# Kernel tuning notes

Hardware: AMD Instinct MI355X
Metric: run time of the kernel (lower is better)

The kernel has to match this reference:

```python
import jax, jax.numpy as jnp
import numpy as np

N, E, FIN, H, OUT, L = 80000, 1280000, 128, 64, 10, 3
NEG_SLOPE = 0.2


def setup_inputs() -> dict:
    key = jax.random.key(0)
    ks = jax.random.split(key, 2 + 6 * L + 2)
    inp = {
        "x": jax.random.normal(ks[0], (N, FIN), dtype=jnp.float32),
        "edge_index": jax.random.randint(ks[1], (2, E), 0, N, dtype=jnp.int32),
        "batch": jnp.zeros((N,), dtype=jnp.int32),
    }
    k = 2
    for l in range(L):
        fin = FIN if l == 0 else H
        s = 1.0 / np.sqrt(fin)
        inp[f"Wl{l}"] = jax.random.normal(ks[k + 0], (H, fin), dtype=jnp.float32) * s
        inp[f"bl{l}"] = jnp.zeros((H,), dtype=jnp.float32)
        inp[f"Wr{l}"] = jax.random.normal(ks[k + 1], (H, fin), dtype=jnp.float32) * s
        inp[f"br{l}"] = jnp.zeros((H,), dtype=jnp.float32)
        inp[f"att{l}"] = jax.random.normal(ks[k + 2], (H,), dtype=jnp.float32) * (1.0 / np.sqrt(H))
        inp[f"b{l}"] = jnp.zeros((H,), dtype=jnp.float32)
        k += 3
    inp["Wro"] = jax.random.normal(ks[k], (OUT, H), dtype=jnp.float32) * (1.0 / np.sqrt(H))
    inp["bro"] = jnp.zeros((OUT,), dtype=jnp.float32)
    return inp


def gatv2_layer(h, src, dst, Wl, bl, Wr, br, att, b):
    # PyG GATv2Conv (heads=1, share_weights=False):
    #   xl = lin_l(h) (source side), xr = lin_r(h) (target side)
    xl = h @ Wl.T + bl          # [N, H]
    xr = h @ Wr.T + br          # [N, H]
    e = jax.nn.leaky_relu(xl[src] + xr[dst], NEG_SLOPE) @ att  # [E_tot]
    # softmax over incoming edges of each destination node
    m = jax.ops.segment_max(e, dst, num_segments=N)
    ex = jnp.exp(e - m[dst])
    denom = jax.ops.segment_sum(ex, dst, num_segments=N)
    alpha = ex / denom[dst]
    out = jax.ops.segment_sum(alpha[:, None] * xl[src], dst, num_segments=N)
    return out + b


def reference(x, edge_index, batch,
              Wl0, bl0, Wr0, br0, att0, b0,
              Wl1, bl1, Wr1, br1, att1, b1,
              Wl2, bl2, Wr2, br2, att2, b2,
              Wro, bro):
    # add self-loops once (same augmented edge set used each layer)
    loop = jnp.arange(N, dtype=edge_index.dtype)
    src = jnp.concatenate([edge_index[0], loop])
    dst = jnp.concatenate([edge_index[1], loop])
    layers = [
        (Wl0, bl0, Wr0, br0, att0, b0),
        (Wl1, bl1, Wr1, br1, att1, b1),
        (Wl2, bl2, Wr2, br2, att2, b2),
    ]
    h = x
    for (Wl, bl, Wr, br, att, b) in layers:
        h = jax.nn.relu(gatv2_layer(h, src, dst, Wl, bl, Wr, br, att, b))
    # graph_level_task=False: node-level readout
    return h @ Wro.T + bro  # [N, OUT]
```

## Files before the change

kernel.cpp:

```cpp
#include <hip/hip_runtime.h>
#include <hip/hip_bf16.h>
#include <hip/hip_fp16.h>


#define NN 80000
#define EE 1280000
#define FIN 128
#define HH 64
#define OUTD 10
#define NBUK 79
#define PCH 2048
#define NCH 625

typedef __hip_bfloat16 bf16;
typedef _Float16 f16x8 __attribute__((ext_vector_type(8)));
typedef float f32x4 __attribute__((ext_vector_type(4)));

__device__ __forceinline__ float ldw(const void* p, int i, int f) {
    return f ? __bfloat162float(((const bf16*)p)[i]) : ((const float*)p)[i];
}

__global__ void detect_kernel(const unsigned* __restrict__ w, int* __restrict__ flag) {
    int lane = threadIdx.x;
    int big = 0;
    for (int i = lane; i < 2048; i += 64) {
        unsigned u = w[i];
        float a = __uint_as_float(u << 16);
        float b = __uint_as_float(u & 0xffff0000u);
        if (!(fabsf(a) <= 1024.f)) big = 1;
        if (!(fabsf(b) <= 1024.f)) big = 1;
    }
    big = (__ballot(big) != 0ull) ? 1 : 0;
    if (lane == 0) flag[0] = big ? 0 : 1;
}

__global__ void preconvert(
    const void* Wl0, const void* Wr0, const void* Wl1, const void* Wr1,
    const void* Wl2, const void* Wr2,
    const void* bl0, const void* br0, const void* bl1, const void* br1,
    const void* bl2, const void* br2,
    const void* att0, const void* att1, const void* att2,
    const void* b0, const void* b1, const void* b2,
    const void* Wro, const void* bro,
    __half* Wh0, __half* Wh1, __half* Wh2, float* small,
    const int* __restrict__ flagp)
{
    const int f = flagp[0];
    int t = blockIdx.x * 256 + threadIdx.x;
    if (t < 16384) {
        int j = t & 127, k = t >> 7;
        float v = (j < 64) ? ldw(Wl0, j * 128 + k, f) : ldw(Wr0, (j - 64) * 128 + k, f);
        Wh0[j * 128 + k] = __float2half(v);
    } else if (t < 24576) {
        int u = t - 16384; int j = u & 127, k = u >> 7;
        float v = (j < 64) ? ldw(Wl1, j * 64 + k, f) : ldw(Wr1, (j - 64) * 64 + k, f);
        Wh1[j * 64 + k] = __float2half(v);
    } else if (t < 32768) {
        int u = t - 24576; int j = u & 127, k = u >> 7;
        float v = (j < 64) ? ldw(Wl2, j * 64 + k, f) : ldw(Wr2, (j - 64) * 64 + k, f);
        Wh2[j * 64 + k] = __float2half(v);
    } else if (t < 34304) {
        int s = t - 32768;
        const void* BL[3] = { bl0, bl1, bl2 };
        const void* BR[3] = { br0, br1, br2 };
        const void* AT[3] = { att0, att1, att2 };
        const void* BB[3] = { b0, b1, b2 };
        float v = 0.f;
        if (s < 384) {
            int l = s / 128, r = s % 128;
            v = (r < 64) ? ldw(BL[l], r, f) : ldw(BR[l], r - 64, f);
        } else if (s < 576) {
            int q = s - 384; v = ldw(AT[q / 64], q % 64, f);
        } else if (s < 768) {
            int q = s - 576; v = ldw(BB[q / 64], q % 64, f);
        } else if (s < 1408) {
            v = ldw(Wro, s - 768, f);
        } else if (s < 1418) {
            v = ldw(bro, s - 1408, f);
        } else return;
        small[s] = v;
    }
}

__global__ __launch_bounds__(256) void chunkhist_kernel(const int* __restrict__ dst,
                                                        int* __restrict__ chunkcnt)
{
    __shared__ int h[NBUK];
    const int tid = threadIdx.x, c = blockIdx.x;
    for (int i = tid; i < NBUK; i += 256) h[i] = 0;
    __syncthreads();
    const int e0 = c * PCH + tid * 8;
    int4 a = *(const int4*)(dst + e0);
    int4 b = *(const int4*)(dst + e0 + 4);
    atomicAdd(&h[a.x >> 10], 1); atomicAdd(&h[a.y >> 10], 1);
    atomicAdd(&h[a.z >> 10], 1); atomicAdd(&h[a.w >> 10], 1);
    atomicAdd(&h[b.x >> 10], 1); atomicAdd(&h[b.y >> 10], 1);
    atomicAdd(&h[b.z >> 10], 1); atomicAdd(&h[b.w >> 10], 1);
    __syncthreads();
    for (int i = tid; i < NBUK; i += 256) chunkcnt[i * NCH + c] = h[i];
}

__global__ __launch_bounds__(1024) void cscan_kernel(int* __restrict__ chunkcnt,
                                                     int* __restrict__ bucket_cnt)
{
    __shared__ int s[1024];
    const int b = blockIdx.x, t = threadIdx.x;
    int v = (t < NCH) ? chunkcnt[b * NCH + t] : 0;
    s[t] = v;
    __syncthreads();
    #pragma unroll
    for (int off = 1; off < 1024; off <<= 1) {
        int u = (t >= off) ? s[t - off] : 0;
        __syncthreads();
        s[t] += u;
        __syncthreads();
    }
    if (t < NCH) chunkcnt[b * NCH + t] = s[t] - v;
    if (t == NCH - 1) bucket_cnt[b] = s[t];
}

__global__ void bscan_kernel(const int* __restrict__ bucket_cnt,
                             int* __restrict__ bucket_base)
{
    __shared__ int sc[128];
    const int t = threadIdx.x;
    sc[t] = (t < NBUK) ? bucket_cnt[t] : 0;
    __syncthreads();
    #pragma unroll
    for (int off = 1; off < 128; off <<= 1) {
        int v = (t >= off) ? sc[t - off] : 0;
        __syncthreads();
        sc[t] += v;
        __syncthreads();
    }
    if (t < NBUK) bucket_base[t] = (t == 0) ? 0 : sc[t - 1];
    if (t == 0) bucket_base[NBUK] = sc[NBUK - 1];
}

__global__ __launch_bounds__(256) void part_kernel(const int* __restrict__ src,
                                                   const int* __restrict__ dst,
                                                   const int* __restrict__ chunkcnt,
                                                   const int* __restrict__ bucket_base,
                                                   int2* __restrict__ part)
{
    __shared__ int hcnt[NBUK];
    __shared__ int sc[128];
    __shared__ int hbase[NBUK + 1];
    __shared__ int hpos[NBUK];
    __shared__ int hgb[NBUK];
    __shared__ int2 stage[PCH];
    const int tid = threadIdx.x, c = blockIdx.x;

    for (int i = tid; i < NBUK; i += 256) hcnt[i] = 0;
    __syncthreads();

    const int e0 = c * PCH + tid * 8;
    int4 sa = *(const int4*)(src + e0);
    int4 sb = *(const int4*)(src + e0 + 4);
    int4 da = *(const int4*)(dst + e0);
    int4 db = *(const int4*)(dst + e0 + 4);
    int dv[8] = { da.x, da.y, da.z, da.w, db.x, db.y, db.z, db.w };
    int sv[8] = { sa.x, sa.y, sa.z, sa.w, sb.x, sb.y, sb.z, sb.w };
    #pragma unroll
    for (int u = 0; u < 8; u++) atomicAdd(&hcnt[dv[u] >> 10], 1);
    __syncthreads();

    if (tid < 128) sc[tid] = (tid < NBUK) ? hcnt[tid] : 0;
    __syncthreads();
    #pragma unroll
    for (int off = 1; off < 128; off <<= 1) {
        int v = (tid < 128 && tid >= off) ? sc[tid - off] : 0;
        __syncthreads();
        if (tid < 128) sc[tid] += v;
        __syncthreads();
    }
    if (tid < NBUK) {
        int b = (tid == 0) ? 0 : sc[tid - 1];
        hbase[tid] = b;
        hpos[tid] = b;
        hgb[tid] = bucket_base[tid] + chunkcnt[tid * NCH + c];
    }
    if (tid == 0) hbase[NBUK] = PCH;
    __syncthreads();

    #pragma unroll
    for (int u = 0; u < 8; u++) {
        int p = atomicAdd(&hpos[dv[u] >> 10], 1);
        stage[p] = make_int2(sv[u], dv[u]);
    }
    __syncthreads();

    for (int s = tid; s < PCH; s += 256) {
        int lo = 0, hi = NBUK;
        #pragma unroll
        for (int it = 0; it < 7; it++) {
            int mid = (lo + hi) >> 1;
            if (hbase[mid] <= s) lo = mid; else hi = mid;
        }
        part[hgb[lo] + (s - hbase[lo])] = stage[s];
    }
}

__global__ __launch_bounds__(256) void hist_part_kernel(const int2* __restrict__ part,
                                                        const int* __restrict__ bucket_base,
                                                        int* __restrict__ cnt)
{
    __shared__ int lcnt[1024];
    const int b = blockIdx.x, tid = threadIdx.x;
    const int dbase = b << 10;
    for (int i = tid; i < 1024; i += 256) lcnt[i] = 0;
    __syncthreads();
    const int eb = bucket_base[b], ee = bucket_base[b + 1];
    for (int e = eb + tid; e < ee; e += 256)
        atomicAdd(&lcnt[part[e].y - dbase], 1);
    __syncthreads();
    const int nd = min(1024, NN - dbase);
    for (int i = tid; i < nd; i += 256) cnt[dbase + i] = lcnt[i];
}

__global__ void scan1(const int* __restrict__ cnt, int* __restrict__ rowptr,
                      int* __restrict__ bsums) {
    __shared__ int sh[256];
    int i = blockIdx.x * 256 + threadIdx.x;
    int tid = threadIdx.x;
    int c = (i < NN) ? cnt[i] : 0;
    sh[tid] = c;
    __syncthreads();
    #pragma unroll
    for (int off = 1; off < 256; off <<= 1) {
        int t = (tid >= off) ? sh[tid - off] : 0;
        __syncthreads();
        sh[tid] += t;
        __syncthreads();
    }
    if (i < NN) rowptr[i + 1] = sh[tid];
    if (tid == 255) bsums[blockIdx.x] = sh[255];
}

__global__ void scan2(int* __restrict__ bsums, int nb) {
    __shared__ int sh[512];
    int t = threadIdx.x;
    sh[t] = (t < nb) ? bsums[t] : 0;
    __syncthreads();
    #pragma unroll
    for (int off = 1; off < 512; off <<= 1) {
        int v = (t >= off) ? sh[t - off] : 0;
        __syncthreads();
        sh[t] += v;
        __syncthreads();
    }
    if (t < nb) bsums[t] = sh[t];
}

__global__ void scan3(int* __restrict__ rowptr, const int* __restrict__ bsums) {
    int i = blockIdx.x * 256 + threadIdx.x;
    if (i == 0) rowptr[0] = 0;
    int add = (blockIdx.x == 0) ? 0 : bsums[blockIdx.x - 1];
    if (i < NN) rowptr[i + 1] += add;
}

__global__ __launch_bounds__(256) void scatter2_kernel(const int2* __restrict__ part,
                                                       const int* __restrict__ bucket_base,
                                                       const int* __restrict__ rowptr,
                                                       int* __restrict__ col)
{
    __shared__ int lfill[1024];
    const int b = blockIdx.x, tid = threadIdx.x;
    const int dbase = b << 10;
    const int nd = min(1024, NN - dbase);
    for (int i = tid; i < nd; i += 256) lfill[i] = rowptr[dbase + i];
    __syncthreads();
    const int eb = bucket_base[b], ee = bucket_base[b + 1];
    for (int e = eb + tid; e < ee; e += 256) {
        int2 sd = part[e];
        int pos = atomicAdd(&lfill[sd.y - dbase], 1);
        col[pos] = sd.x;
    }
}

#define ELX_S 72
#define EXR_S 68
template<int F, bool L0>
__global__ __launch_bounds__(256) void lin_mfma(const void* __restrict__ hin_,
                                                const __half* __restrict__ Wh,
                                                const float* __restrict__ biasLR,
                                                const float* __restrict__ attf,
                                                __half* __restrict__ xlh,
                                                float* __restrict__ xr,
                                                float* __restrict__ slp,
                                                float* __restrict__ srp,
                                                const int* __restrict__ flagp)
{
    __shared__ __align__(16) char lds[64 * ELX_S * 2 + 64 * EXR_S * 4];
    _Float16* xs  = (_Float16*)lds;
    _Float16* eXL = (_Float16*)lds;
    float*    eXR = (float*)(lds + 64 * ELX_S * 2);

    const int tid = threadIdx.x;
    const int nb = blockIdx.x * 64;
    constexpr int OPR = F / 8;

    if (L0 && flagp[0]) {
        const uint4* hp = (const uint4*)hin_;
        for (int c = tid; c < 64 * OPR; c += 256) {
            int row = c / OPR, oct = c % OPR;
            uint4 u = hp[((size_t)(nb + row) * F + oct * 8) >> 3];
            unsigned ww[4] = { u.x, u.y, u.z, u.w };
            _Float16 v[8];
            #pragma unroll
            for (int p = 0; p < 4; p++) {
                v[2 * p]     = (_Float16)__uint_as_float(ww[p] << 16);
                v[2 * p + 1] = (_Float16)__uint_as_float(ww[p] & 0xffff0000u);
            }
            int so = oct ^ (row & 7);
            *(f16x8*)&xs[row * F + so * 8] = *(f16x8*)v;
        }
    } else {
        const float4* hp = (const float4*)hin_;
        for (int c = tid; c < 64 * OPR; c += 256) {
            int row = c / OPR, oct = c % OPR;
            size_t base = ((size_t)(nb + row) * F + oct * 8) >> 2;
            float4 a = hp[base], b = hp[base + 1];
            _Float16 v[8] = { (_Float16)a.x, (_Float16)a.y, (_Float16)a.z, (_Float16)a.w,
                              (_Float16)b.x, (_Float16)b.y, (_Float16)b.z, (_Float16)b.w };
            int so = oct ^ (row & 7);
            *(f16x8*)&xs[row * F + so * 8] = *(f16x8*)v;
        }
    }
    __syncthreads();

    const int w = tid >> 6;
    const int lane = tid & 63;
    const int n = lane & 15;
    const int quad = lane >> 4;
    constexpr int NS = F / 32;

    f16x8 afr[NS];
    #pragma unroll
    for (int s = 0; s < NS; s++) {
        int o = (s * 4 + quad) ^ (n & 7);
        afr[s] = *(const f16x8*)&xs[(w * 16 + n) * F + o * 8];
    }
    __syncthreads();

    const _Float16* Whf = (const _Float16*)Wh;
    #pragma unroll
    for (int ct = 0; ct < 8; ct++) {
        float bv = biasLR[ct * 16 + n];
        f32x4 acc = { bv, bv, bv, bv };
        #pragma unroll
        for (int s = 0; s < NS; s++) {
            f16x8 bfr = *(const f16x8*)&Whf[(size_t)(ct * 16 + n) * F + s * 32 + quad * 8];
            acc = __builtin_amdgcn_mfma_f32_16x16x32_f16(afr[s], bfr, acc, 0, 0, 0);
        }
        int rbase = w * 16 + quad * 4;
        if (ct < 4) {
            #pragma unroll
            for (int rg = 0; rg < 4; rg++)
                eXL[(rbase + rg) * ELX_S + ct * 16 + n] = (_Float16)acc[rg];
        } else {
            #pragma unroll
            for (int rg = 0; rg < 4; rg++)
                eXR[(rbase + rg) * EXR_S + (ct - 4) * 16 + n] = acc[rg];
        }
    }
    __syncthreads();

    for (int c = tid; c < 512; c += 256) {
        int row = c >> 3, oct = c & 7;
        *(uint4*)&xlh[(size_t)(nb + row) * 64 + oct * 8] =
            *(const uint4*)&eXL[row * ELX_S + oct * 8];
    }
    for (int c = tid; c < 1024; c += 256) {
        int row = c >> 4, q4 = c & 15;
        *(float4*)&xr[(size_t)(nb + row) * 64 + q4 * 4] =
            *(const float4*)&eXR[row * EXR_S + q4 * 4];
    }

    if (tid < 64) {
        float accl = 0.f, accr = 0.f;
        #pragma unroll
        for (int o = 0; o < 8; o++) {
            f16x8 vl = *(const f16x8*)&eXL[tid * ELX_S + o * 8];
            float4 a0 = *(const float4*)(attf + o * 8);
            float4 a1 = *(const float4*)(attf + o * 8 + 4);
            float4 v0 = *(const float4*)&eXR[tid * EXR_S + o * 8];
            float4 v1 = *(const float4*)&eXR[tid * EXR_S + o * 8 + 4];
            accl = fmaf(a0.x, (float)vl[0], accl);
            accl = fmaf(a0.y, (float)vl[1], accl);
            accl = fmaf(a0.z, (float)vl[2], accl);
            accl = fmaf(a0.w, (float)vl[3], accl);
            accl = fmaf(a1.x, (float)vl[4], accl);
            accl = fmaf(a1.y, (float)vl[5], accl);
            accl = fmaf(a1.z, (float)vl[6], accl);
            accl = fmaf(a1.w, (float)vl[7], accl);
            accr = fmaf(a0.x, v0.x, accr);
            accr = fmaf(a0.y, v0.y, accr);
            accr = fmaf(a0.z, v0.z, accr);
            accr = fmaf(a0.w, v0.w, accr);
            accr = fmaf(a1.x, v1.x, accr);
            accr = fmaf(a1.y, v1.y, accr);
            accr = fmaf(a1.z, v1.z, accr);
            accr = fmaf(a1.w, v1.w, accr);
        }
        slp[nb + tid] = accl;
        srp[nb + tid] = accr;
    }
}

#define DECODE8(U, D) { \
    float2 _f0 = __half22float2(*(__half2*)&U.x); \
    float2 _f1 = __half22float2(*(__half2*)&U.y); \
    float2 _f2 = __half22float2(*(__half2*)&U.z); \
    float2 _f3 = __half22float2(*(__half2*)&U.w); \
    D[0]=_f0.x; D[1]=_f0.y; D[2]=_f1.x; D[3]=_f1.y; \
    D[4]=_f2.x; D[5]=_f2.y; D[6]=_f3.x; D[7]=_f3.y; }

__global__ __launch_bounds__(256) void agg5_kernel(const __half* __restrict__ xlh,
                                                   const float* __restrict__ xr,
                                                   const float* __restrict__ slp,
                                                   const float* __restrict__ srp,
                                                   const float* __restrict__ attf,
                                                   const float* __restrict__ bf,
                                                   const int* __restrict__ rowptr,
                                                   const int* __restrict__ col,
                                                   float* __restrict__ hout)
{
    const int lane = threadIdx.x & 63;
    const int g = lane >> 3;
    const int r = lane & 7;
    int iw = blockIdx.x * 4 + (threadIdx.x >> 6);
    if (iw >= NN) return;
    const int i = __builtin_amdgcn_readfirstlane(iw);

    float xri[8], att[8];
    {
        float4 xa = *(const float4*)(xr + (size_t)i * 64 + r * 8);
        float4 xb = *(const float4*)(xr + (size_t)i * 64 + r * 8 + 4);
        xri[0]=xa.x; xri[1]=xa.y; xri[2]=xa.z; xri[3]=xa.w;
        xri[4]=xb.x; xri[5]=xb.y; xri[6]=xb.z; xri[7]=xb.w;
        float4 aa = *(const float4*)(attf + r * 8);
        float4 ab = *(const float4*)(attf + r * 8 + 4);
        att[0]=aa.x; att[1]=aa.y; att[2]=aa.z; att[3]=aa.w;
        att[4]=ab.x; att[5]=ab.y; att[6]=ab.z; att[7]=ab.w;
    }
    const float sri06 = 0.6f * srp[i];

    uint4 srow = *(const uint4*)(xlh + (size_t)i * 64 + r * 8);
    float s[8]; DECODE8(srow, s);
    float ps = 0.f;
    #pragma unroll
    for (int k = 0; k < 8; k++)
        ps = fmaf(att[k], fabsf(s[k] + xri[k]), ps);
    ps += __shfl_xor(ps, 1, 64);
    ps += __shfl_xor(ps, 2, 64);
    ps += __shfl_xor(ps, 4, 64);
    float es = fmaf(0.4f, ps, fmaf(0.6f, slp[i], sri06));
    float wself = __expf(fminf(es, 60.f));

    float acc[8];
    float denom;
    if (g == 0) {
        #pragma unroll
        for (int k = 0; k < 8; k++) acc[k] = wself * s[k];
        denom = wself;
    } else {
        #pragma unroll
        for (int k = 0; k < 8; k++) acc[k] = 0.f;
        denom = 0.f;
    }

    const int e0 = rowptr[i], e1 = rowptr[i + 1];
    const int n = e1 - e0;
    const int nfull = n & ~15;

    int base = 0;
    for (; base < nfull; base += 16) {
        const int j = e0 + base;
        int sa = col[j + g];
        int sb = col[j + 8 + g];
        float sla = slp[sa], slb = slp[sb];
        uint4 ua = *(const uint4*)(xlh + (size_t)sa * 64 + r * 8);
        uint4 ub = *(const uint4*)(xlh + (size_t)sb * 64 + r * 8);
        float A[8], B[8];
        DECODE8(ua, A);
        DECODE8(ub, B);

        float pa = 0.f, pb = 0.f;
        #pragma unroll
        for (int k = 0; k < 8; k++) {
            pa = fmaf(att[k], fabsf(A[k] + xri[k]), pa);
            pb = fmaf(att[k], fabsf(B[k] + xri[k]), pb);
        }
        pa += __shfl_xor(pa, 1, 64);  pb += __shfl_xor(pb, 1, 64);
        pa += __shfl_xor(pa, 2, 64);  pb += __shfl_xor(pb, 2, 64);
        pa += __shfl_xor(pa, 4, 64);  pb += __shfl_xor(pb, 4, 64);

        float ea = fmaf(0.4f, pa, fmaf(0.6f, sla, sri06));
        float eb = fmaf(0.4f, pb, fmaf(0.6f, slb, sri06));
        float wa = __expf(fminf(ea, 60.f));
        float wb = __expf(fminf(eb, 60.f));

        #pragma unroll
        for (int k = 0; k < 8; k++) {
            acc[k] = fmaf(wa, A[k], acc[k]);
            acc[k] = fmaf(wb, B[k], acc[k]);
        }
        denom += wa + wb;
    }

    const int rem = n - base;
    if (rem > 0) {
        const int j = e0 + base;
        const int eL = e1 - 1;
        if (rem > 8) {
            int sa = col[j + g];
            int sb = col[min(j + 8 + g, eL)];
            float sla = slp[sa], slb = slp[sb];
            uint4 ua = *(const uint4*)(xlh + (size_t)sa * 64 + r * 8);
            uint4 ub = *(const uint4*)(xlh + (size_t)sb * 64 + r * 8);
            float A[8], B[8];
            DECODE8(ua, A);
            DECODE8(ub, B);

            float pa = 0.f, pb = 0.f;
            #pragma unroll
            for (int k = 0; k < 8; k++) {
                pa = fmaf(att[k], fabsf(A[k] + xri[k]), pa);
                pb = fmaf(att[k], fabsf(B[k] + xri[k]), pb);
            }
            pa += __shfl_xor(pa, 1, 64);  pb += __shfl_xor(pb, 1, 64);
            pa += __shfl_xor(pa, 2, 64);  pb += __shfl_xor(pb, 2, 64);
            pa += __shfl_xor(pa, 4, 64);  pb += __shfl_xor(pb, 4, 64);

            float ea = fmaf(0.4f, pa, fmaf(0.6f, sla, sri06));
            float eb = fmaf(0.4f, pb, fmaf(0.6f, slb, sri06));
            float wa = __expf(fminf(ea, 60.f));
            float wb = (8 + g < rem) ? __expf(fminf(eb, 60.f)) : 0.f;

            #pragma unroll
            for (int k = 0; k < 8; k++) {
                acc[k] = fmaf(wa, A[k], acc[k]);
                acc[k] = fmaf(wb, B[k], acc[k]);
            }
            denom += wa + wb;
        } else {
            int sa = col[min(j + g, eL)];
            float sla = slp[sa];
            uint4 ua = *(const uint4*)(xlh + (size_t)sa * 64 + r * 8);
            float A[8];
            DECODE8(ua, A);

            float pa = 0.f;
            #pragma unroll
            for (int k = 0; k < 8; k++)
                pa = fmaf(att[k], fabsf(A[k] + xri[k]), pa);
            pa += __shfl_xor(pa, 1, 64);
            pa += __shfl_xor(pa, 2, 64);
            pa += __shfl_xor(pa, 4, 64);

            float ea = fmaf(0.4f, pa, fmaf(0.6f, sla, sri06));
            float wa = (g < rem) ? __expf(fminf(ea, 60.f)) : 0.f;

            #pragma unroll
            for (int k = 0; k < 8; k++)
                acc[k] = fmaf(wa, A[k], acc[k]);
            denom += wa;
        }
    }

    #pragma unroll
    for (int off = 8; off < 64; off <<= 1) {
        #pragma unroll
        for (int k = 0; k < 8; k++) acc[k] += __shfl_xor(acc[k], off, 64);
        denom += __shfl_xor(denom, off, 64);
    }

    if (g == 0) {
        float inv = 1.f / denom;
        float4 bfa = *(const float4*)(bf + r * 8);
        float4 bfb = *(const float4*)(bf + r * 8 + 4);
        float o0 = fmaxf(fmaf(acc[0], inv, bfa.x), 0.f);
        float o1 = fmaxf(fmaf(acc[1], inv, bfa.y), 0.f);
        float o2 = fmaxf(fmaf(acc[2], inv, bfa.z), 0.f);
        float o3 = fmaxf(fmaf(acc[3], inv, bfa.w), 0.f);
        float o4 = fmaxf(fmaf(acc[4], inv, bfb.x), 0.f);
        float o5 = fmaxf(fmaf(acc[5], inv, bfb.y), 0.f);
        float o6 = fmaxf(fmaf(acc[6], inv, bfb.z), 0.f);
        float o7 = fmaxf(fmaf(acc[7], inv, bfb.w), 0.f);
        float* op = hout + (size_t)i * 64 + r * 8;
        *(float4*)(op)     = make_float4(o0, o1, o2, o3);
        *(float4*)(op + 4) = make_float4(o4, o5, o6, o7);
    }
}

__global__ __launch_bounds__(256) void readout2_kernel(const float* __restrict__ h,
                                                       const float* __restrict__ WROf,
                                                       const float* __restrict__ brof,
                                                       void* __restrict__ out,
                                                       const int* __restrict__ flagp)
{
    __shared__ float wsh[640];
    __shared__ float bsh[OUTD];
    const int tid = threadIdx.x;
    for (int idx = tid; idx < 640; idx += 256) {
        int k = idx / 10, o = idx % 10;
        wsh[idx] = WROf[o * 64 + k];
    }
    if (tid < OUTD) bsh[tid] = brof[tid];
    __syncthreads();

    const int i = blockIdx.x * 256 + tid;
    if (i >= NN) return;
    const int f = flagp[0];

    float res[OUTD];
    #pragma unroll
    for (int o = 0; o < OUTD; o++) res[o] = bsh[o];

    const float4* h4 = (const float4*)(h + (size_t)i * 64);
    #pragma unroll 4
    for (int c = 0; c < 16; c++) {
        float4 hv = h4[c];
        const float* wp = &wsh[c * 40];
        #pragma unroll
        for (int o = 0; o < OUTD; o++) {
            float t = fmaf(hv.x, wp[o], fmaf(hv.y, wp[10 + o],
                      fmaf(hv.z, wp[20 + o], hv.w * wp[30 + o])));
            res[o] += t;
        }
    }

    if (f) {
        bf16* op = (bf16*)out + (size_t)i * OUTD;
        #pragma unroll
        for (int o = 0; o < OUTD; o++) op[o] = __float2bfloat16(res[o]);
    } else {
        float* op = (float*)out + (size_t)i * OUTD;
        #pragma unroll
        for (int o = 0; o < OUTD; o++) op[o] = res[o];
    }
}

extern "C" void kernel_launch(void* const* d_in, const int* in_sizes, int n_in,
                              void* d_out, int out_size, void* d_ws, size_t ws_size,
                              hipStream_t stream) {
    const void* x   = d_in[0];
    const int* ei   = (const int*)d_in[1];
    const void* Wl0 = d_in[3];  const void* bl0 = d_in[4];
    const void* Wr0 = d_in[5];  const void* br0 = d_in[6];
    const void* at0 = d_in[7];  const void* b0  = d_in[8];
    const void* Wl1 = d_in[9];  const void* bl1 = d_in[10];
    const void* Wr1 = d_in[11]; const void* br1 = d_in[12];
    const void* at1 = d_in[13]; const void* b1  = d_in[14];
    const void* Wl2 = d_in[15]; const void* bl2 = d_in[16];
    const void* Wr2 = d_in[17]; const void* br2 = d_in[18];
    const void* at2 = d_in[19]; const void* b2  = d_in[20];
    const void* Wro = d_in[21]; const void* bro = d_in[22];

    const int* srcArr = ei;
    const int* dstArr = ei + EE;

    float* wf = (float*)d_ws;
    __half* Wh0  = (__half*)wf;
    __half* Wh1  = (__half*)(wf + 16384);
    __half* Wh2  = (__half*)(wf + 24576);
    float* small = wf + 32768;
    int*   flag  = (int*)(wf + 34304);
    int*   rowptr = (int*)(wf + 34368);
    int*   bsums  = (int*)(wf + 114496);
    int*   fillc  = (int*)(wf + 115008);
    int*   bucket_cnt  = (int*)(wf + 195008);
    int*   bucket_base = (int*)(wf + 195136);
    int*   chunkcnt    = (int*)(wf + 195264);
    int2*  part   = (int2*)(wf + 244736);
    int*   col    = (int*)(wf + 2804736);
    float* slp    = wf + 4084736;
    float* srp    = wf + 4164736;
    __half* xlh   = (__half*)(wf + 5364736);
    float* xr = wf + 7924736;
    float* hA = xr + (size_t)NN * 64;

    float* biasLR0 = small;        float* biasLR1 = small + 128; float* biasLR2 = small + 256;
    float* attf0 = small + 384;    float* attf1 = small + 448;   float* attf2 = small + 512;
    float* bf0   = small + 576;    float* bf1   = small + 640;   float* bf2   = small + 704;
    float* WROf  = small + 768;    float* brof  = small + 1408;

    detect_kernel<<<dim3(1), dim3(64), 0, stream>>>((const unsigned*)Wl0, flag);

    preconvert<<<dim3(134), dim3(256), 0, stream>>>(
        Wl0, Wr0, Wl1, Wr1, Wl2, Wr2, bl0, br0, bl1, br1, bl2, br2,
        at0, at1, at2, b0, b1, b2, Wro, bro, Wh0, Wh1, Wh2, small, flag);

    chunkhist_kernel<<<dim3(NCH), dim3(256), 0, stream>>>(dstArr, chunkcnt);
    cscan_kernel<<<dim3(NBUK), dim3(1024), 0, stream>>>(chunkcnt, bucket_cnt);
    bscan_kernel<<<dim3(1), dim3(128), 0, stream>>>(bucket_cnt, bucket_base);
    part_kernel<<<dim3(NCH), dim3(256), 0, stream>>>(srcArr, dstArr, chunkcnt, bucket_base, part);
    hist_part_kernel<<<dim3(NBUK), dim3(256), 0, stream>>>(part, bucket_base, fillc);
    scan1<<<dim3(313), dim3(256), 0, stream>>>(fillc, rowptr, bsums);
    scan2<<<dim3(1), dim3(512), 0, stream>>>(bsums, 313);
    scan3<<<dim3(313), dim3(256), 0, stream>>>(rowptr, bsums);
    scatter2_kernel<<<dim3(NBUK), dim3(256), 0, stream>>>(part, bucket_base, rowptr, col);

    lin_mfma<128, true><<<dim3(NN / 64), dim3(256), 0, stream>>>(x, Wh0, biasLR0, attf0, xlh, xr, slp, srp, flag);
    agg5_kernel<<<dim3(NN / 4), dim3(256), 0, stream>>>(xlh, xr, slp, srp, attf0, bf0, rowptr, col, hA);
    lin_mfma<64, false><<<dim3(NN / 64), dim3(256), 0, stream>>>(hA, Wh1, biasLR1, attf1, xlh, xr, slp, srp, flag);
    agg5_kernel<<<dim3(NN / 4), dim3(256), 0, stream>>>(xlh, xr, slp, srp, attf1, bf1, rowptr, col, hA);
    lin_mfma<64, false><<<dim3(NN / 64), dim3(256), 0, stream>>>(hA, Wh2, biasLR2, attf2, xlh, xr, slp, srp, flag);
    agg5_kernel<<<dim3(NN / 4), dim3(256), 0, stream>>>(xlh, xr, slp, srp, attf2, bf2, rowptr, col, hA);

    readout2_kernel<<<dim3(313), dim3(256), 0, stream>>>(hA, WROf, brof, d_out, flag);
}
```

Measured before the change: 402.2 us.

## Map eight destination nodes per wavefront with 8-lane groups in aggregation

The aggregation kernel now gives each 8-lane group its own destination node, so a wavefront handles eight nodes, instead of spreading one node's edges across all 64 lanes. Each group walks its node's edge list two at a time, which removes the cross-group shuffle reduction and the masked tail handling. The risk is divergence and load imbalance across groups whose nodes have different degrees, plus less memory-level parallelism per node.

```diff
diff --git a/kernel.cpp b/kernel.cpp
--- a/kernel.cpp
+++ b/kernel.cpp
@@ -416,7 +416,7 @@
     D[0]=_f0.x; D[1]=_f0.y; D[2]=_f1.x; D[3]=_f1.y; \
     D[4]=_f2.x; D[5]=_f2.y; D[6]=_f3.x; D[7]=_f3.y; }
 
-__global__ __launch_bounds__(256) void agg5_kernel(const __half* __restrict__ xlh,
+__global__ __launch_bounds__(256) void agg6_kernel(const __half* __restrict__ xlh,
                                                    const float* __restrict__ xr,
                                                    const float* __restrict__ slp,
                                                    const float* __restrict__ srp,
@@ -429,9 +429,8 @@
     const int lane = threadIdx.x & 63;
     const int g = lane >> 3;
     const int r = lane & 7;
-    int iw = blockIdx.x * 4 + (threadIdx.x >> 6);
-    if (iw >= NN) return;
-    const int i = __builtin_amdgcn_readfirstlane(iw);
+    const int wid = blockIdx.x * 4 + (threadIdx.x >> 6);
+    const int i = wid * 8 + g;
 
     float xri[8], att[8];
     {
@@ -459,26 +458,16 @@
     float wself = __expf(fminf(es, 60.f));
 
     float acc[8];
-    float denom;
-    if (g == 0) {
-        #pragma unroll
-        for (int k = 0; k < 8; k++) acc[k] = wself * s[k];
-        denom = wself;
-    } else {
-        #pragma unroll
-        for (int k = 0; k < 8; k++) acc[k] = 0.f;
-        denom = 0.f;
-    }
+    #pragma unroll
+    for (int k = 0; k < 8; k++) acc[k] = wself * s[k];
+    float denom = wself;
 
     const int e0 = rowptr[i], e1 = rowptr[i + 1];
-    const int n = e1 - e0;
-    const int nfull = n & ~15;
-
-    int base = 0;
-    for (; base < nfull; base += 16) {
-        const int j = e0 + base;
-        int sa = col[j + g];
-        int sb = col[j + 8 + g];
+
+    int e = e0;
+    for (; e + 2 <= e1; e += 2) {
+        int sa = col[e];
+        int sb = col[e + 1];
         float sla = slp[sa], slb = slp[sb];
         uint4 ua = *(const uint4*)(xlh + (size_t)sa * 64 + r * 8);
         uint4 ub = *(const uint4*)(xlh + (size_t)sb * 64 + r * 8);
@@ -508,90 +497,44 @@
         }
         denom += wa + wb;
     }
-
-    const int rem = n - base;
-    if (rem > 0) {
-        const int j = e0 + base;
-        const int eL = e1 - 1;
-        if (rem > 8) {
-            int sa = col[j + g];
-            int sb = col[min(j + 8 + g, eL)];
-            float sla = slp[sa], slb = slp[sb];
-            uint4 ua = *(const uint4*)(xlh + (size_t)sa * 64 + r * 8);
-            uint4 ub = *(const uint4*)(xlh + (size_t)sb * 64 + r * 8);
-            float A[8], B[8];
-            DECODE8(ua, A);
-            DECODE8(ub, B);
-
-            float pa = 0.f, pb = 0.f;
-            #pragma unroll
-            for (int k = 0; k < 8; k++) {
-                pa = fmaf(att[k], fabsf(A[k] + xri[k]), pa);
-                pb = fmaf(att[k], fabsf(B[k] + xri[k]), pb);
-            }
-            pa += __shfl_xor(pa, 1, 64);  pb += __shfl_xor(pb, 1, 64);
-            pa += __shfl_xor(pa, 2, 64);  pb += __shfl_xor(pb, 2, 64);
-            pa += __shfl_xor(pa, 4, 64);  pb += __shfl_xor(pb, 4, 64);
-
-            float ea = fmaf(0.4f, pa, fmaf(0.6f, sla, sri06));
-            float eb = fmaf(0.4f, pb, fmaf(0.6f, slb, sri06));
-            float wa = __expf(fminf(ea, 60.f));
-            float wb = (8 + g < rem) ? __expf(fminf(eb, 60.f)) : 0.f;
-
-            #pragma unroll
-            for (int k = 0; k < 8; k++) {
-                acc[k] = fmaf(wa, A[k], acc[k]);
-                acc[k] = fmaf(wb, B[k], acc[k]);
-            }
-            denom += wa + wb;
-        } else {
-            int sa = col[min(j + g, eL)];
-            float sla = slp[sa];
-            uint4 ua = *(const uint4*)(xlh + (size_t)sa * 64 + r * 8);
-            float A[8];
-            DECODE8(ua, A);
-
-            float pa = 0.f;
-            #pragma unroll
-            for (int k = 0; k < 8; k++)
-                pa = fmaf(att[k], fabsf(A[k] + xri[k]), pa);
-            pa += __shfl_xor(pa, 1, 64);
-            pa += __shfl_xor(pa, 2, 64);
-            pa += __shfl_xor(pa, 4, 64);
-
-            float ea = fmaf(0.4f, pa, fmaf(0.6f, sla, sri06));
-            float wa = (g < rem) ? __expf(fminf(ea, 60.f)) : 0.f;
-
-            #pragma unroll
-            for (int k = 0; k < 8; k++)
-                acc[k] = fmaf(wa, A[k], acc[k]);
-            denom += wa;
-        }
-    }
-
-    #pragma unroll
-    for (int off = 8; off < 64; off <<= 1) {
-        #pragma unroll
-        for (int k = 0; k < 8; k++) acc[k] += __shfl_xor(acc[k], off, 64);
-        denom += __shfl_xor(denom, off, 64);
-    }
-
-    if (g == 0) {
-        float inv = 1.f / denom;
-        float4 bfa = *(const float4*)(bf + r * 8);
-        float4 bfb = *(const float4*)(bf + r * 8 + 4);
-        float o0 = fmaxf(fmaf(acc[0], inv, bfa.x), 0.f);
-        float o1 = fmaxf(fmaf(acc[1], inv, bfa.y), 0.f);
-        float o2 = fmaxf(fmaf(acc[2], inv, bfa.z), 0.f);
-        float o3 = fmaxf(fmaf(acc[3], inv, bfa.w), 0.f);
-        float o4 = fmaxf(fmaf(acc[4], inv, bfb.x), 0.f);
-        float o5 = fmaxf(fmaf(acc[5], inv, bfb.y), 0.f);
-        float o6 = fmaxf(fmaf(acc[6], inv, bfb.z), 0.f);
-        float o7 = fmaxf(fmaf(acc[7], inv, bfb.w), 0.f);
-        float* op = hout + (size_t)i * 64 + r * 8;
-        *(float4*)(op)     = make_float4(o0, o1, o2, o3);
-        *(float4*)(op + 4) = make_float4(o4, o5, o6, o7);
-    }
+    if (e < e1) {
+        int sa = col[e];
+        float sla = slp[sa];
+        uint4 ua = *(const uint4*)(xlh + (size_t)sa * 64 + r * 8);
+        float A[8];
+        DECODE8(ua, A);
+
+        float pa = 0.f;
+        #pragma unroll
+        for (int k = 0; k < 8; k++)
+            pa = fmaf(att[k], fabsf(A[k] + xri[k]), pa);
+        pa += __shfl_xor(pa, 1, 64);
+        pa += __shfl_xor(pa, 2, 64);
+        pa += __shfl_xor(pa, 4, 64);
+
+        float ea = fmaf(0.4f, pa, fmaf(0.6f, sla, sri06));
+        float wa = __expf(fminf(ea, 60.f));
+
+        #pragma unroll
+        for (int k = 0; k < 8; k++)
+            acc[k] = fmaf(wa, A[k], acc[k]);
+        denom += wa;
+    }
+
+    float inv = 1.f / denom;
+    float4 bfa = *(const float4*)(bf + r * 8);
+    float4 bfb = *(const float4*)(bf + r * 8 + 4);
+    float o0 = fmaxf(fmaf(acc[0], inv, bfa.x), 0.f);
+    float o1 = fmaxf(fmaf(acc[1], inv, bfa.y), 0.f);
+    float o2 = fmaxf(fmaf(acc[2], inv, bfa.z), 0.f);
+    float o3 = fmaxf(fmaf(acc[3], inv, bfa.w), 0.f);
+    float o4 = fmaxf(fmaf(acc[4], inv, bfb.x), 0.f);
+    float o5 = fmaxf(fmaf(acc[5], inv, bfb.y), 0.f);
+    float o6 = fmaxf(fmaf(acc[6], inv, bfb.z), 0.f);
+    float o7 = fmaxf(fmaf(acc[7], inv, bfb.w), 0.f);
+    float* op = hout + (size_t)i * 64 + r * 8;
+    *(float4*)(op)     = make_float4(o0, o1, o2, o3);
+    *(float4*)(op + 4) = make_float4(o4, o5, o6, o7);
 }
 
 __global__ __launch_bounds__(256) void readout2_kernel(const float* __restrict__ h,
@@ -703,11 +646,11 @@
     scatter2_kernel<<<dim3(NBUK), dim3(256), 0, stream>>>(part, bucket_base, rowptr, col);
 
     lin_mfma<128, true><<<dim3(NN / 64), dim3(256), 0, stream>>>(x, Wh0, biasLR0, attf0, xlh, xr, slp, srp, flag);
-    agg5_kernel<<<dim3(NN / 4), dim3(256), 0, stream>>>(xlh, xr, slp, srp, attf0, bf0, rowptr, col, hA);
+    agg6_kernel<<<dim3(NN / 32), dim3(256), 0, stream>>>(xlh, xr, slp, srp, attf0, bf0, rowptr, col, hA);
     lin_mfma<64, false><<<dim3(NN / 64), dim3(256), 0, stream>>>(hA, Wh1, biasLR1, attf1, xlh, xr, slp, srp, flag);
-    agg5_kernel<<<dim3(NN / 4), dim3(256), 0, stream>>>(xlh, xr, slp, srp, attf1, bf1, rowptr, col, hA);
+    agg6_kernel<<<dim3(NN / 32), dim3(256), 0, stream>>>(xlh, xr, slp, srp, attf1, bf1, rowptr, col, hA);
     lin_mfma<64, false><<<dim3(NN / 64), dim3(256), 0, stream>>>(hA, Wh2, biasLR2, attf2, xlh, xr, slp, srp, flag);
-    agg5_kernel<<<dim3(NN / 4), dim3(256), 0, stream>>>(xlh, xr, slp, srp, attf2, bf2, rowptr, col, hA);
+    agg6_kernel<<<dim3(NN / 32), dim3(256), 0, stream>>>(xlh, xr, slp, srp, attf2, bf2, rowptr, col, hA);
 
     readout2_kernel<<<dim3(313), dim3(256), 0, stream>>>(hA, WROf, brof, d_out, flag);
 }
```

Measured after the change: 379.4 us. 5.7% less time.
